# Kernel optimization log

Measured on AMD Instinct MI355X. Metric: run time of the kernel, lower is better.

Reference implementation:

```python
import jax, jax.numpy as jnp
import numpy as np

B, C, H, W, HEADS = 16, 256, 64, 64, 4
BN_EPS = 1e-5


def setup_inputs() -> dict:
    key = jax.random.key(0)
    ks = jax.random.split(key, 6)
    sc = lambda k, shape, s: (jax.random.normal(k, shape, jnp.float32) * s)
    return {
        "x": sc(ks[0], (B, C, H, W), 1.0),
        "qkv_w": sc(ks[1], (C, C), C ** -0.5),
        "temp": jnp.ones((HEADS, 1), jnp.float32),
        "proj_w": sc(ks[2], (C, C), C ** -0.5),
        "proj_b": jnp.zeros((C,), jnp.float32),
        "conv1_w": sc(ks[3], (2 * C, C), C ** -0.5),
        "bn1_g": jnp.ones((2 * C,), jnp.float32),
        "bn1_b": jnp.zeros((2 * C,), jnp.float32),
        "bn1_m": jnp.zeros((2 * C,), jnp.float32),
        "bn1_v": jnp.ones((2 * C,), jnp.float32),
        "conv2_w": sc(ks[4], (C, 2 * C), (2 * C) ** -0.5),
        "bn2_g": jnp.ones((C,), jnp.float32),
        "bn2_b": jnp.zeros((C,), jnp.float32),
        "bn2_m": jnp.zeros((C,), jnp.float32),
        "bn2_v": jnp.ones((C,), jnp.float32),
    }


def _attention_tssa(x3, qkv_w, temp, proj_w, proj_b):
    # x3: [b, n, c]
    b, n, c = x3.shape
    d = c // HEADS
    w = (x3 @ qkv_w.T).reshape(b, n, HEADS, d).transpose(0, 2, 1, 3)  # b h n d
    # F.normalize over token dim (dim=-2), eps=1e-12
    nrm = jnp.sqrt(jnp.sum(w * w, axis=2, keepdims=True))
    w_normed = w / jnp.maximum(nrm, 1e-12)
    # logits [b, h, n]; temp is (h, 1) -> broadcast per head
    s = jnp.sum(w_normed * w_normed, axis=-1) * temp[:, 0][None, :, None]
    Pi = jax.nn.softmax(s, axis=1)  # softmax over HEAD dim (torch Softmax(dim=1))
    Pi_n = Pi / (jnp.sum(Pi, axis=-1, keepdims=True) + 1e-8)
    dots = jnp.einsum('bhn,bhnd->bhd', Pi_n, w * w)  # [b, h, d]
    attn = 1.0 / (1.0 + dots)
    out = -(w * Pi[..., None]) * attn[:, :, None, :]  # b h n d
    out = out.transpose(0, 2, 1, 3).reshape(b, n, c)
    return out @ proj_w.T + proj_b


def _bn(y, g, b_, m, v):
    scale = (g / jnp.sqrt(v + BN_EPS))[None, :, None, None]
    return (y - m[None, :, None, None]) * scale + b_[None, :, None, None]


def reference(x, qkv_w, temp, proj_w, proj_b, conv1_w, bn1_g, bn1_b, bn1_m, bn1_v,
              conv2_w, bn2_g, bn2_b, bn2_m, bn2_v):
    b, c, h, w_ = x.shape
    x3 = x.reshape(b, c, h * w_).transpose(0, 2, 1)  # b n c
    a = _attention_tssa(x3, qkv_w, temp, proj_w, proj_b)  # b n c
    x = x + a.transpose(0, 2, 1).reshape(b, c, h, w_)
    # FFN: 1x1 conv -> BN -> SiLU -> 1x1 conv -> BN (no act), residual
    y = jnp.einsum('bchw,oc->bohw', x, conv1_w)
    y = _bn(y, bn1_g, bn1_b, bn1_m, bn1_v)
    y = y * jax.nn.sigmoid(y)  # SiLU
    z = jnp.einsum('bchw,oc->bohw', y, conv2_w)
    z = _bn(z, bn2_g, bn2_b, bn2_m, bn2_v)
    return x + z
```

## Files before the change

kernel.cpp:

```cpp
#include <hip/hip_runtime.h>
#include <hip/hip_bf16.h>
#include <stdint.h>

typedef unsigned short u16;
using bf16x8 = __attribute__((ext_vector_type(8))) short;
using f32x4  = __attribute__((ext_vector_type(4))) float;

#define DEVI static __device__ __forceinline__
#define AS1 __attribute__((address_space(1)))
#define AS3 __attribute__((address_space(3)))

constexpr int CB = 16;
constexpr int CC = 256;
constexpr int CN = 4096;
constexpr int CH = 4;

DEVI u16 f2b(float f){
  union { float f; uint32_t u; } v; v.f = f;
  return (u16)((v.u + 0x7FFFu + ((v.u >> 16) & 1u)) >> 16);
}
DEVI float b2f(u16 u){
  union { uint32_t u; float f; } v; v.u = ((uint32_t)u) << 16; return v.f;
}

__global__ __launch_bounds__(256) void k_prep_w(const float* __restrict__ qkv, const float* __restrict__ pj,
    const float* __restrict__ c1, const float* __restrict__ c2,
    u16* __restrict__ qkvb, u16* __restrict__ pjb, u16* __restrict__ c1b, u16* __restrict__ c2b){
  int id = blockIdx.x * 256 + threadIdx.x;
  if (id < 65536) qkvb[id] = f2b(qkv[id]);
  else if (id < 131072) pjb[id - 65536] = f2b(pj[id - 65536]);
  else if (id < 262144) c1b[id - 131072] = f2b(c1[id - 131072]);
  else c2b[id - 262144] = f2b(c2[id - 262144]);
}

__global__ __launch_bounds__(256) void k_prep_bn(const float* __restrict__ g1,const float* __restrict__ b1,
    const float* __restrict__ m1,const float* __restrict__ v1,
    const float* __restrict__ g2,const float* __restrict__ b2,
    const float* __restrict__ m2,const float* __restrict__ v2,
    float* __restrict__ s1,float* __restrict__ o1,float* __restrict__ s2,float* __restrict__ o2){
  int id = blockIdx.x*256 + threadIdx.x;
  if (id < 512){ float s = g1[id] * rsqrtf(v1[id] + 1e-5f); s1[id] = s; o1[id] = b1[id] - m1[id]*s; }
  else if (id < 768){ int c = id - 512; float s = g2[c] * rsqrtf(v2[c] + 1e-5f); s2[c] = s; o2[c] = b2[c] - m2[c]*s; }
}

__global__ __launch_bounds__(256) void k_tr(const float* __restrict__ x, u16* __restrict__ xb){
  __shared__ float t[32][33];
  int b = blockIdx.x, c0 = blockIdx.y*32, n0 = blockIdx.z*32;
  int tr = threadIdx.x >> 5, tc = threadIdx.x & 31;
  const float* xp = x + ((size_t)b*CC + c0)*CN + n0;
  #pragma unroll
  for (int p=0;p<4;p++) t[tr + p*8][tc] = xp[(size_t)(tr + p*8)*CN + tc];
  __syncthreads();
  u16* op = xb + ((size_t)b*CN + n0)*CC + c0;
  #pragma unroll
  for (int p=0;p<4;p++) op[(size_t)(tr + p*8)*CC + tc] = f2b(t[tc][tr + p*8]);
}

template<int M_, int K_, int EPI>
__global__ __launch_bounds__(256) void k_gemm(
    const u16* __restrict__ Aw, const u16* __restrict__ Act,
    float* of, u16* __restrict__ ob,
    const float* __restrict__ e0, const float* __restrict__ e1,
    const u16* __restrict__ eb)
{
  __shared__ __align__(16) u16 smem[16384];
  u16* As = smem;
  u16* Bs = smem + 8192;
  const int t = threadIdx.x;
  const int lane = t & 63, wave = t >> 6;
  const int wr = wave >> 1, wc = wave & 1;
  const int lg = lane >> 4, lr = lane & 15;
  const int gx = gridDim.x, gy = gridDim.y;
  const int nwg = gx * gy * gridDim.z;
  const int id0 = blockIdx.x + gx*(blockIdx.y + gy*blockIdx.z);
  const int id  = (id0 & 7)*(nwg >> 3) + (id0 >> 3);
  const int bx = id % gx; const int rem = id / gx;
  const int by = rem % gy; const int bz = rem / gy;
  const int n0 = bx * 128, m0 = by * 128, b = bz;
  const u16* Ag = Aw + (size_t)m0 * K_;
  const u16* Bg = Act + ((size_t)b * CN + n0) * K_;
  f32x4 acc[4][4] = {};
  constexpr int NT = K_/32;
  int goff[2], ldst[2];
  #pragma unroll
  for (int i=0;i<2;i++){
    int off = (i*256 + t) * 8;
    int row = off >> 5, kq = (off >> 3) & 3;
    goff[i] = row*K_ + (kq ^ (row & 3)) * 8;
    ldst[i] = off;
  }
  auto stage = [&](int p, int kt){
    #pragma unroll
    for (int i=0;i<2;i++){
      __builtin_amdgcn_global_load_lds((AS1 void*)(Ag + goff[i] + kt*32),
                                       (AS3 void*)(As + p*4096 + ldst[i]), 16, 0, 0);
      __builtin_amdgcn_global_load_lds((AS1 void*)(Bg + goff[i] + kt*32),
                                       (AS3 void*)(Bs + p*4096 + ldst[i]), 16, 0, 0);
    }
  };
  stage(0, 0);
  stage(1, 1);
  for (int kt = 0; kt < NT; ++kt){
    const int cur = kt & 1;
    if (kt + 1 < NT) { asm volatile("s_waitcnt vmcnt(4)" ::: "memory"); }
    else             { asm volatile("s_waitcnt vmcnt(0)" ::: "memory"); }
    __builtin_amdgcn_s_barrier();
    __builtin_amdgcn_sched_barrier(0);
    bf16x8 af[4], bfv[4];
    #pragma unroll
    for (int mi=0;mi<4;mi++){
      int r = wr*64 + mi*16 + lr;
      af[mi] = *(const bf16x8*)(As + cur*4096 + r*32 + ((lg ^ (r & 3)) * 8));
      int r2 = wc*64 + mi*16 + lr;
      bfv[mi] = *(const bf16x8*)(Bs + cur*4096 + r2*32 + ((lg ^ (r2 & 3)) * 8));
    }
    asm volatile("s_waitcnt lgkmcnt(0)" ::: "memory");
    __builtin_amdgcn_sched_barrier(0);
    __builtin_amdgcn_s_barrier();
    if (kt + 2 < NT) stage(cur, kt + 2);
    __builtin_amdgcn_s_setprio(1);
    #pragma unroll
    for (int mi=0;mi<4;mi++)
      #pragma unroll
      for (int ni=0;ni<4;ni++)
        acc[mi][ni] = __builtin_amdgcn_mfma_f32_16x16x32_bf16(af[mi], bfv[ni], acc[mi][ni], 0, 0, 0);
    __builtin_amdgcn_s_setprio(0);
  }
  #pragma unroll
  for (int mi=0;mi<4;mi++){
    const int mb = m0 + wr*64 + mi*16 + lg*4;
    float sq[4] = {0.f,0.f,0.f,0.f};
    #pragma unroll
    for (int ni=0;ni<4;ni++){
      const int n = n0 + wc*64 + ni*16 + lr;
      f32x4 v = acc[mi][ni];
      if constexpr (EPI == 0){
        ushort4 u;
        #pragma unroll
        for (int j=0;j<4;j++){ ((u16*)&u)[j] = f2b(v[j]); sq[j] += v[j]*v[j]; }
        *(ushort4*)(ob + ((size_t)b*CN + n)*M_ + mb) = u;
      } else if constexpr (EPI == 1){
        ushort4 xw = *(const ushort4*)(eb + ((size_t)b*CN + n)*M_ + mb);
        ushort4 u;
        #pragma unroll
        for (int j=0;j<4;j++)
          ((u16*)&u)[j] = f2b(v[j] + e0[mb + j] + b2f(((const u16*)&xw)[j]));
        *(ushort4*)(ob + ((size_t)b*CN + n)*M_ + mb) = u;
      } else if constexpr (EPI == 2){
        ushort4 u;
        #pragma unroll
        for (int j=0;j<4;j++){
          float r = v[j]*e0[mb+j] + e1[mb+j];
          r = r / (1.f + __expf(-r));
          ((u16*)&u)[j] = f2b(r);
        }
        *(ushort4*)(ob + ((size_t)b*CN + n)*M_ + mb) = u;
      } else {
        ushort4 xw = *(const ushort4*)(eb + ((size_t)b*CN + n)*M_ + mb);
        #pragma unroll
        for (int j=0;j<4;j++){
          size_t ix = ((size_t)b*CC + mb + j)*CN + n;
          of[ix] = v[j]*e0[mb+j] + e1[mb+j] + b2f(((const u16*)&xw)[j]);
        }
      }
    }
    if constexpr (EPI == 0){
      #pragma unroll
      for (int off=1; off<16; off<<=1)
        #pragma unroll
        for (int j=0;j<4;j++) sq[j] += __shfl_xor(sq[j], off);
      if (lr == 0){
        #pragma unroll
        for (int j=0;j<4;j++) atomicAdd(&of[b*CC + mb + j], sq[j]);
      }
    }
  }
}

__global__ __launch_bounds__(256) void k_stats(const u16* __restrict__ W, const float* __restrict__ nrm2,
    const float* __restrict__ temp, float* __restrict__ Pi, float* __restrict__ sumPi,
    float* __restrict__ dotsU){
  __shared__ float red[4][256];
  const int b = blockIdx.x, n0 = blockIdx.y * 64;
  const int t = threadIdx.x, lane = t & 63, wave = t >> 6;
  const int grp = lane >> 4, gl = lane & 15;
  const float th = temp[grp];
  const float4 nr = *(const float4*)(nrm2 + b*CC + 4*lane);
  const float i0 = 1.f/fmaxf(nr.x,1e-24f), i1 = 1.f/fmaxf(nr.y,1e-24f);
  const float i2 = 1.f/fmaxf(nr.z,1e-24f), i3 = 1.f/fmaxf(nr.w,1e-24f);
  float accp = 0.f, d0=0.f, d1=0.f, d2=0.f, d3=0.f;
  for (int i=0;i<16;i++){
    int n = n0 + wave*16 + i;
    ushort4 wu = *(const ushort4*)(W + ((size_t)b*CN + n)*CC + 4*lane);
    float w0=b2f(wu.x), w1=b2f(wu.y), w2=b2f(wu.z), w3=b2f(wu.w);
    float q0=w0*w0, q1=w1*w1, q2=w2*w2, q3=w3*w3;
    float s = q0*i0 + q1*i1 + q2*i2 + q3*i3;
    #pragma unroll
    for (int off=1; off<16; off<<=1) s += __shfl_xor(s, off);
    s *= th;
    float sA=__shfl(s,0), sB=__shfl(s,16), sC=__shfl(s,32), sD=__shfl(s,48);
    float mx = fmaxf(fmaxf(sA,sB), fmaxf(sC,sD));
    float eA=__expf(sA-mx), eB=__expf(sB-mx), eC=__expf(sC-mx), eD=__expf(sD-mx);
    float den = eA+eB+eC+eD;
    float pih = ((grp==0)?eA:(grp==1)?eB:(grp==2)?eC:eD)/den;
    if (gl == 0){ Pi[((size_t)b*CH + grp)*CN + n] = pih; accp += pih; }
    d0 += pih*q0; d1 += pih*q1; d2 += pih*q2; d3 += pih*q3;
  }
  if (gl == 0) atomicAdd(&sumPi[b*CH + grp], accp);
  red[wave][4*lane+0]=d0; red[wave][4*lane+1]=d1; red[wave][4*lane+2]=d2; red[wave][4*lane+3]=d3;
  __syncthreads();
  float sm = red[0][t]+red[1][t]+red[2][t]+red[3][t];
  atomicAdd(&dotsU[b*CC + t], sm);
}

__global__ __launch_bounds__(256) void k_outc(const u16* __restrict__ W, const float* __restrict__ Pi,
    const float* __restrict__ dotsU, const float* __restrict__ sumPi, u16* __restrict__ oc){
  size_t id = (size_t)blockIdx.x * 256 + threadIdx.x;
  int c = ((int)(id & 63)) * 4;
  int n = (int)((id >> 6) & (CN - 1));
  int b = (int)(id >> 18);
  int h = c >> 6;
  ushort4 wu = *(const ushort4*)(W + ((size_t)b*CN + n)*CC + c);
  float pi = Pi[((size_t)b*CH + h)*CN + n];
  float sp = sumPi[b*CH + h] + 1e-8f;
  float4 du = *(const float4*)(dotsU + b*CC + c);
  float a0 = sp/(sp + du.x), a1 = sp/(sp + du.y), a2 = sp/(sp + du.z), a3 = sp/(sp + du.w);
  ushort4 u;
  u.x = f2b(-b2f(wu.x) * pi * a0);
  u.y = f2b(-b2f(wu.y) * pi * a1);
  u.z = f2b(-b2f(wu.z) * pi * a2);
  u.w = f2b(-b2f(wu.w) * pi * a3);
  *(ushort4*)(oc + ((size_t)b*CN + n)*CC + c) = u;
}

extern "C" void kernel_launch(void* const* d_in, const int* in_sizes, int n_in,
                              void* d_out, int out_size, void* d_ws, size_t ws_size,
                              hipStream_t stream) {
  (void)in_sizes; (void)n_in; (void)out_size; (void)ws_size;
  const float* x     = (const float*)d_in[0];
  const float* qkvw  = (const float*)d_in[1];
  const float* temp  = (const float*)d_in[2];
  const float* projw = (const float*)d_in[3];
  const float* projb = (const float*)d_in[4];
  const float* c1w   = (const float*)d_in[5];
  const float* g1=(const float*)d_in[6], *b1=(const float*)d_in[7], *m1=(const float*)d_in[8], *v1=(const float*)d_in[9];
  const float* c2w   = (const float*)d_in[10];
  const float* g2=(const float*)d_in[11], *b2=(const float*)d_in[12], *m2=(const float*)d_in[13], *v2=(const float*)d_in[14];
  float* out = (float*)d_out;
  char* ws = (char*)d_ws;

  constexpr size_t MB = 1024*1024;
  u16* xb  = (u16*)(ws);
  u16* oc  = (u16*)(ws + 32*MB);
  u16* yb  = (u16*)(ws);
  u16* xrb = (u16*)(ws + 64*MB);
  u16* Wb  = (u16*)(ws + 96*MB);
  char* wts = ws + 128*MB;
  u16* qkvb = (u16*)wts;
  u16* pjb  = qkvb + 65536;
  u16* c1b  = pjb + 65536;
  u16* c2b  = c1b + 131072;
  float* s1 = (float*)(wts + 786432);
  float* o1 = s1 + 512;
  float* s2 = o1 + 512;
  float* o2 = s2 + 256;
  float* Pi = (float*)(wts + 786432 + 8192);
  float* nrm2  = Pi + (size_t)CB*CH*CN;
  float* sumPi = nrm2 + CB*CC;
  float* dotsU = sumPi + CB*CH;

  hipMemsetAsync(nrm2, 0, (size_t)(CB*CC + CB*CH + CB*CC)*4, stream);
  k_prep_w<<<1536, 256, 0, stream>>>(qkvw, projw, c1w, c2w, qkvb, pjb, c1b, c2b);
  k_prep_bn<<<3, 256, 0, stream>>>(g1,b1,m1,v1,g2,b2,m2,v2,s1,o1,s2,o2);
  k_tr<<<dim3(CB, CC/32, CN/32), 256, 0, stream>>>(x, xb);
  k_gemm<256,256,0><<<dim3(CN/128, 2, CB), 256, 0, stream>>>(qkvb, xb, nrm2, Wb, nullptr, nullptr, nullptr);
  k_stats<<<dim3(CB, CN/64), 256, 0, stream>>>(Wb, nrm2, temp, Pi, sumPi, dotsU);
  k_outc<<<(CB*CN*CC/4)/256, 256, 0, stream>>>(Wb, Pi, dotsU, sumPi, oc);
  k_gemm<256,256,1><<<dim3(CN/128, 2, CB), 256, 0, stream>>>(pjb, oc, nullptr, xrb, projb, nullptr, xb);
  k_gemm<512,256,2><<<dim3(CN/128, 4, CB), 256, 0, stream>>>(c1b, xrb, nullptr, yb, s1, o1, nullptr);
  k_gemm<256,512,3><<<dim3(CN/128, 2, CB), 256, 0, stream>>>(c2b, yb, out, nullptr, s2, o2, xrb);
}
```

Before: 242.7 us.

## Replace LDS-staged GEMM pipeline with direct global-to-register MFMA operand loads

Removes the shared-memory double buffer, the global_load_lds staging and the per-step barriers from the bf16 GEMM kernel. Each wave now loads its MFMA fragments straight from global memory into registers, with the K loop fully unrolled. This drops the LDS traffic and synchronisation cost, but loses data sharing between waves, so each operand is fetched from global or L2 several times, and the loads become 16-byte strided per lane.

```diff
diff --git a/kernel.cpp b/kernel.cpp
--- a/kernel.cpp
+++ b/kernel.cpp
@@ -7,8 +7,6 @@
 using f32x4  = __attribute__((ext_vector_type(4))) float;
 
 #define DEVI static __device__ __forceinline__
-#define AS1 __attribute__((address_space(1)))
-#define AS3 __attribute__((address_space(3)))
 
 constexpr int CB = 16;
 constexpr int CC = 256;
@@ -63,9 +61,6 @@
     const float* __restrict__ e0, const float* __restrict__ e1,
     const u16* __restrict__ eb)
 {
-  __shared__ __align__(16) u16 smem[16384];
-  u16* As = smem;
-  u16* Bs = smem + 8192;
   const int t = threadIdx.x;
   const int lane = t & 63, wave = t >> 6;
   const int wr = wave >> 1, wc = wave & 1;
@@ -77,54 +72,26 @@
   const int bx = id % gx; const int rem = id / gx;
   const int by = rem % gy; const int bz = rem / gy;
   const int n0 = bx * 128, m0 = by * 128, b = bz;
-  const u16* Ag = Aw + (size_t)m0 * K_;
-  const u16* Bg = Act + ((size_t)b * CN + n0) * K_;
+  const u16* pa[4]; const u16* pb[4];
+  #pragma unroll
+  for (int mi=0;mi<4;mi++)
+    pa[mi] = Aw + (size_t)(m0 + wr*64 + mi*16 + lr)*K_ + lg*8;
+  #pragma unroll
+  for (int ni=0;ni<4;ni++)
+    pb[ni] = Act + ((size_t)b*CN + n0 + wc*64 + ni*16 + lr)*K_ + lg*8;
   f32x4 acc[4][4] = {};
-  constexpr int NT = K_/32;
-  int goff[2], ldst[2];
-  #pragma unroll
-  for (int i=0;i<2;i++){
-    int off = (i*256 + t) * 8;
-    int row = off >> 5, kq = (off >> 3) & 3;
-    goff[i] = row*K_ + (kq ^ (row & 3)) * 8;
-    ldst[i] = off;
-  }
-  auto stage = [&](int p, int kt){
-    #pragma unroll
-    for (int i=0;i<2;i++){
-      __builtin_amdgcn_global_load_lds((AS1 void*)(Ag + goff[i] + kt*32),
-                                       (AS3 void*)(As + p*4096 + ldst[i]), 16, 0, 0);
-      __builtin_amdgcn_global_load_lds((AS1 void*)(Bg + goff[i] + kt*32),
-                                       (AS3 void*)(Bs + p*4096 + ldst[i]), 16, 0, 0);
-    }
-  };
-  stage(0, 0);
-  stage(1, 1);
-  for (int kt = 0; kt < NT; ++kt){
-    const int cur = kt & 1;
-    if (kt + 1 < NT) { asm volatile("s_waitcnt vmcnt(4)" ::: "memory"); }
-    else             { asm volatile("s_waitcnt vmcnt(0)" ::: "memory"); }
-    __builtin_amdgcn_s_barrier();
-    __builtin_amdgcn_sched_barrier(0);
-    bf16x8 af[4], bfv[4];
-    #pragma unroll
-    for (int mi=0;mi<4;mi++){
-      int r = wr*64 + mi*16 + lr;
-      af[mi] = *(const bf16x8*)(As + cur*4096 + r*32 + ((lg ^ (r & 3)) * 8));
-      int r2 = wc*64 + mi*16 + lr;
-      bfv[mi] = *(const bf16x8*)(Bs + cur*4096 + r2*32 + ((lg ^ (r2 & 3)) * 8));
-    }
-    asm volatile("s_waitcnt lgkmcnt(0)" ::: "memory");
-    __builtin_amdgcn_sched_barrier(0);
-    __builtin_amdgcn_s_barrier();
-    if (kt + 2 < NT) stage(cur, kt + 2);
-    __builtin_amdgcn_s_setprio(1);
+  #pragma unroll
+  for (int tt=0; tt<K_/32; ++tt){
+    bf16x8 af[4], bv[4];
+    #pragma unroll
+    for (int mi=0;mi<4;mi++) af[mi] = *(const bf16x8*)(pa[mi] + tt*32);
+    #pragma unroll
+    for (int ni=0;ni<4;ni++) bv[ni] = *(const bf16x8*)(pb[ni] + tt*32);
     #pragma unroll
     for (int mi=0;mi<4;mi++)
       #pragma unroll
       for (int ni=0;ni<4;ni++)
-        acc[mi][ni] = __builtin_amdgcn_mfma_f32_16x16x32_bf16(af[mi], bfv[ni], acc[mi][ni], 0, 0, 0);
-    __builtin_amdgcn_s_setprio(0);
+        acc[mi][ni] = __builtin_amdgcn_mfma_f32_16x16x32_bf16(af[mi], bv[ni], acc[mi][ni], 0, 0, 0);
   }
   #pragma unroll
   for (int mi=0;mi<4;mi++){
```

Measured after the change: 334.6 us. 1.38x slower.
